# Kernel tuning notes

Measured on AMD Instinct MI355X. Metric: run time of the kernel, lower is better.

## Reference

```python
import jax, jax.numpy as jnp
import numpy as np

BT, L, F, N = 8, 8192, 128, 16


def setup_inputs() -> dict:
    key = jax.random.key(0)
    ks = jax.random.split(key, 7)
    scale = 1.0 / np.sqrt(F)
    x = jax.random.normal(ks[0], (BT, L, F), dtype=jnp.float32)
    Wb = jax.random.normal(ks[1], (F, N), dtype=jnp.float32) * scale
    bb = jax.random.normal(ks[2], (N,), dtype=jnp.float32) * 0.01
    Wc = jax.random.normal(ks[3], (F, N), dtype=jnp.float32) * scale
    bc = jax.random.normal(ks[4], (N,), dtype=jnp.float32) * 0.01
    Wd = jax.random.normal(ks[5], (F, 1), dtype=jnp.float32) * scale
    bd = jax.random.normal(ks[6], (1,), dtype=jnp.float32) * 0.01
    # diagonal HiPPO-like spectrum (A is diagonal in the source: torch.diag(eigenvalues))
    A = -(jnp.arange(N, dtype=jnp.float32) + 1.0)
    return {"x": x, "Wb": Wb, "bb": bb, "Wc": Wc, "bc": bc, "Wd": Wd, "bd": bd, "A": A}


def reference(x, Wb, bb, Wc, bc, Wd, bd, A):
    # input-dependent SSM parameters (S6 / selective scan)
    B = x @ Wb + bb                      # [BT, L, N]
    C = x @ Wc + bc                      # [BT, L, N]
    delta = jax.nn.softplus(x @ Wd + bd)  # [BT, L, 1]
    # ZOH discretization with diagonal A
    dA = jnp.exp(delta * A)              # [BT, L, N]
    dB = (dA - 1.0) / A * B              # [BT, L, N]

    def step(h, inp):
        dA_t, dB_t, x_t, C_t = inp       # [BT,N],[BT,N],[BT,F],[BT,N]
        # h: [BT, F, N]; each feature channel has its own N-dim state
        h = dA_t[:, None, :] * h + dB_t[:, None, :] * x_t[:, :, None]
        y = jnp.einsum('bfn,bn->bf', h, C_t)
        return h, y

    h0 = jnp.zeros((x.shape[0], x.shape[2], A.shape[0]), dtype=x.dtype)
    xs = (jnp.swapaxes(dA, 0, 1), jnp.swapaxes(dB, 0, 1),
          jnp.swapaxes(x, 0, 1), jnp.swapaxes(C, 0, 1))
    _, ys = jax.lax.scan(step, h0, xs)   # ys: [L, BT, F]
    return jnp.swapaxes(ys, 0, 1)        # [BT, L, F]
```

## Files before the change

kernel.cpp:

```cpp
#include <hip/hip_runtime.h>


#define BTc   8
#define Lseq  8192
#define Fdim  128
#define Ndim  16
#define CH    128
#define LC    64

__global__ __launch_bounds__(256) void k_pre(
    const float* __restrict__ x,
    const float* __restrict__ Wb, const float* __restrict__ bb,
    const float* __restrict__ Wc, const float* __restrict__ bc,
    const float* __restrict__ Wd, const float* __restrict__ bd,
    const float* __restrict__ A,  float* __restrict__ G)
{
    __shared__ float Wl[33][128];
    int tid = threadIdx.x;
    for (int idx = tid; idx < 33 * 128; idx += 256) {
        int j = idx >> 7, k = idx & 127;
        float v;
        if (j < 16)      v = Wb[k * 16 + j];
        else if (j < 32) v = Wc[k * 16 + (j - 16)];
        else             v = Wd[k];
        Wl[j][k] = v;
    }
    __syncthreads();

    int token = blockIdx.x * 256 + tid;
    const float* xr = x + (size_t)token * 128;

    float acc[33];
#pragma unroll
    for (int j = 0; j < 33; j++) acc[j] = 0.f;

#pragma unroll 2
    for (int kk = 0; kk < 32; kk++) {
        float4 xv = reinterpret_cast<const float4*>(xr)[kk];
#pragma unroll
        for (int j = 0; j < 33; j++) {
            float4 w = *reinterpret_cast<const float4*>(&Wl[j][kk * 4]);
            acc[j] = fmaf(xv.x, w.x, acc[j]);
            acc[j] = fmaf(xv.y, w.y, acc[j]);
            acc[j] = fmaf(xv.z, w.z, acc[j]);
            acc[j] = fmaf(xv.w, w.w, acc[j]);
        }
    }

    float v = acc[32] + bd[0];
    float delta = fmaxf(v, 0.f) + log1pf(expf(-fabsf(v)));

    float out[48];
#pragma unroll
    for (int n = 0; n < 16; n++) {
        float An = A[n];
        float Bn = acc[n] + bb[n];
        float Cn = acc[16 + n] + bc[n];
        float dA = expf(delta * An);
        float dB = (dA - 1.f) / An * Bn;
        out[n]      = dA;
        out[16 + n] = dB;
        out[32 + n] = Cn;
    }
    float4* Gr = reinterpret_cast<float4*>(G + (size_t)token * 48);
#pragma unroll
    for (int q = 0; q < 12; q++)
        Gr[q] = make_float4(out[4*q], out[4*q+1], out[4*q+2], out[4*q+3]);
}

__global__ __launch_bounds__(128) void k_local(
    const float* __restrict__ x, const float* __restrict__ G,
    float* __restrict__ q, float* __restrict__ P)
{
    __shared__ float Gl[LC][48];
    int c = blockIdx.x, b = blockIdx.y;
    int f = threadIdx.x;
    int t0 = c * LC;
    const float* Gc = G + (size_t)(b * Lseq + t0) * 48;
    for (int idx = f; idx < LC * 48 / 4; idx += 128)
        reinterpret_cast<float4*>(&Gl[0][0])[idx] =
            reinterpret_cast<const float4*>(Gc)[idx];
    __syncthreads();

    float h[16], pr[16];
#pragma unroll
    for (int n = 0; n < 16; n++) { h[n] = 0.f; pr[n] = 1.f; }

    const float* xp = x + (size_t)(b * Lseq + t0) * 128 + f;
    for (int t = 0; t < LC; t++) {
        float xv = xp[t * 128];
#pragma unroll
        for (int n = 0; n < 16; n++) {
            float dA = Gl[t][n];
            float dB = Gl[t][16 + n];
            h[n]  = fmaf(dA, h[n], dB * xv);
            pr[n] *= dA;
        }
    }

    float* qp = q + ((size_t)(b * CH + c) * 128 + f) * 16;
#pragma unroll
    for (int n = 0; n < 16; n++) qp[n] = h[n];
    if (f == 0) {
        float* Pp = P + (size_t)(b * CH + c) * 16;
#pragma unroll
        for (int n = 0; n < 16; n++) Pp[n] = pr[n];
    }
}

__global__ __launch_bounds__(256) void k_chunkscan(
    const float* __restrict__ q, const float* __restrict__ P,
    float* __restrict__ Hin)
{
    int id = blockIdx.x * 256 + threadIdx.x;
    int b  = id >> 11;
    int fn = id & 2047;
    int n  = id & 15;
    float H = 0.f;
    for (int c = 0; c < CH; c++) {
        size_t base = (size_t)(b * CH + c);
        Hin[base * 2048 + fn] = H;
        float Pc = P[base * 16 + n];
        float qc = q[base * 2048 + fn];
        H = fmaf(Pc, H, qc);
    }
}

__global__ __launch_bounds__(128) void k_final(
    const float* __restrict__ x, const float* __restrict__ G,
    const float* __restrict__ Hin, float* __restrict__ y)
{
    __shared__ float Gl[LC][48];
    int c = blockIdx.x, b = blockIdx.y;
    int f = threadIdx.x;
    int t0 = c * LC;
    const float* Gc = G + (size_t)(b * Lseq + t0) * 48;
    for (int idx = f; idx < LC * 48 / 4; idx += 128)
        reinterpret_cast<float4*>(&Gl[0][0])[idx] =
            reinterpret_cast<const float4*>(Gc)[idx];
    __syncthreads();

    float h[16];
    const float* hp = Hin + ((size_t)(b * CH + c) * 128 + f) * 16;
#pragma unroll
    for (int n = 0; n < 16; n++) h[n] = hp[n];

    const float* xp = x + (size_t)(b * Lseq + t0) * 128 + f;
    float*       yp = y + (size_t)(b * Lseq + t0) * 128 + f;
    for (int t = 0; t < LC; t++) {
        float xv  = xp[t * 128];
        float acc = 0.f;
#pragma unroll
        for (int n = 0; n < 16; n++) {
            float dA = Gl[t][n];
            float dB = Gl[t][16 + n];
            float Cn = Gl[t][32 + n];
            h[n] = fmaf(dA, h[n], dB * xv);
            acc  = fmaf(Cn, h[n], acc);
        }
        yp[t * 128] = acc;
    }
}

extern "C" void kernel_launch(void* const* d_in, const int* in_sizes, int n_in,
                              void* d_out, int out_size, void* d_ws, size_t ws_size,
                              hipStream_t stream) {
    const float* x  = (const float*)d_in[0];
    const float* Wb = (const float*)d_in[1];
    const float* bb = (const float*)d_in[2];
    const float* Wc = (const float*)d_in[3];
    const float* bc = (const float*)d_in[4];
    const float* Wd = (const float*)d_in[5];
    const float* bd = (const float*)d_in[6];
    const float* A  = (const float*)d_in[7];
    float* y = (float*)d_out;

    float* G   = (float*)d_ws;
    float* q   = G   + (size_t)BTc * Lseq * 48;
    float* P   = q   + (size_t)BTc * CH * Fdim * Ndim;
    float* Hin = P   + (size_t)BTc * CH * Ndim;

    k_pre<<<dim3(BTc * Lseq / 256), 256, 0, stream>>>(x, Wb, bb, Wc, bc, Wd, bd, A, G);
    k_local<<<dim3(CH, BTc), 128, 0, stream>>>(x, G, q, P);
    k_chunkscan<<<dim3(BTc * Fdim * Ndim / 256), 256, 0, stream>>>(q, P, Hin);
    k_final<<<dim3(CH, BTc), 128, 0, stream>>>(x, G, Hin, y);
}
```

Measured before the change: 95.84 us.

## Fuse projection with local chunk scan and replace final rescan with linear correction

New measurement: 119.6 us. 1.25x slower.

```diff
diff --git a/kernel.cpp b/kernel.cpp
--- a/kernel.cpp
+++ b/kernel.cpp
@@ -8,15 +8,29 @@
 #define CH    128
 #define LC    64
 
-__global__ __launch_bounds__(256) void k_pre(
+__global__ __launch_bounds__(256) void k_fused_local(
     const float* __restrict__ x,
     const float* __restrict__ Wb, const float* __restrict__ bb,
     const float* __restrict__ Wc, const float* __restrict__ bc,
     const float* __restrict__ Wd, const float* __restrict__ bd,
-    const float* __restrict__ A,  float* __restrict__ G)
+    const float* __restrict__ A,
+    float* __restrict__ y,
+    float* __restrict__ q, float* __restrict__ P, float* __restrict__ E)
 {
+    __shared__ float Xl[LC][132];
     __shared__ float Wl[33][128];
-    int tid = threadIdx.x;
+    __shared__ float Gl[LC][48];
+    __shared__ float El[LC][16];
+
+    const int tid = threadIdx.x;
+    const int c = blockIdx.x, b = blockIdx.y;
+    const size_t tok0 = (size_t)b * Lseq + (size_t)c * LC;
+
+    const float4* xg = reinterpret_cast<const float4*>(x + tok0 * Fdim);
+    for (int idx = tid; idx < LC * 32; idx += 256) {
+        int t = idx >> 5, k4 = idx & 31;
+        *reinterpret_cast<float4*>(&Xl[t][k4 * 4]) = xg[idx];
+    }
     for (int idx = tid; idx < 33 * 128; idx += 256) {
         int j = idx >> 7, k = idx & 127;
         float v;
@@ -27,84 +41,80 @@
     }
     __syncthreads();
 
-    int token = blockIdx.x * 256 + tid;
-    const float* xr = x + (size_t)token * 128;
-
-    float acc[33];
-#pragma unroll
-    for (int j = 0; j < 33; j++) acc[j] = 0.f;
-
-#pragma unroll 2
-    for (int kk = 0; kk < 32; kk++) {
-        float4 xv = reinterpret_cast<const float4*>(xr)[kk];
-#pragma unroll
-        for (int j = 0; j < 33; j++) {
-            float4 w = *reinterpret_cast<const float4*>(&Wl[j][kk * 4]);
-            acc[j] = fmaf(xv.x, w.x, acc[j]);
-            acc[j] = fmaf(xv.y, w.y, acc[j]);
-            acc[j] = fmaf(xv.z, w.z, acc[j]);
-            acc[j] = fmaf(xv.w, w.w, acc[j]);
-        }
-    }
-
-    float v = acc[32] + bd[0];
-    float delta = fmaxf(v, 0.f) + log1pf(expf(-fabsf(v)));
-
-    float out[48];
-#pragma unroll
-    for (int n = 0; n < 16; n++) {
-        float An = A[n];
-        float Bn = acc[n] + bb[n];
-        float Cn = acc[16 + n] + bc[n];
-        float dA = expf(delta * An);
-        float dB = (dA - 1.f) / An * Bn;
-        out[n]      = dA;
-        out[16 + n] = dB;
-        out[32 + n] = Cn;
-    }
-    float4* Gr = reinterpret_cast<float4*>(G + (size_t)token * 48);
-#pragma unroll
-    for (int q = 0; q < 12; q++)
-        Gr[q] = make_float4(out[4*q], out[4*q+1], out[4*q+2], out[4*q+3]);
-}
-
-__global__ __launch_bounds__(128) void k_local(
-    const float* __restrict__ x, const float* __restrict__ G,
-    float* __restrict__ q, float* __restrict__ P)
-{
-    __shared__ float Gl[LC][48];
-    int c = blockIdx.x, b = blockIdx.y;
-    int f = threadIdx.x;
-    int t0 = c * LC;
-    const float* Gc = G + (size_t)(b * Lseq + t0) * 48;
-    for (int idx = f; idx < LC * 48 / 4; idx += 128)
-        reinterpret_cast<float4*>(&Gl[0][0])[idx] =
-            reinterpret_cast<const float4*>(Gc)[idx];
-    __syncthreads();
-
-    float h[16], pr[16];
-#pragma unroll
-    for (int n = 0; n < 16; n++) { h[n] = 0.f; pr[n] = 1.f; }
-
-    const float* xp = x + (size_t)(b * Lseq + t0) * 128 + f;
-    for (int t = 0; t < LC; t++) {
-        float xv = xp[t * 128];
-#pragma unroll
-        for (int n = 0; n < 16; n++) {
-            float dA = Gl[t][n];
-            float dB = Gl[t][16 + n];
-            h[n]  = fmaf(dA, h[n], dB * xv);
-            pr[n] *= dA;
-        }
-    }
-
-    float* qp = q + ((size_t)(b * CH + c) * 128 + f) * 16;
-#pragma unroll
-    for (int n = 0; n < 16; n++) qp[n] = h[n];
-    if (f == 0) {
-        float* Pp = P + (size_t)(b * CH + c) * 16;
-#pragma unroll
-        for (int n = 0; n < 16; n++) Pp[n] = pr[n];
+    {
+        const int t = tid >> 2, ks = tid & 3;
+        float acc[33];
+#pragma unroll
+        for (int j = 0; j < 33; ++j) acc[j] = 0.f;
+#pragma unroll
+        for (int kk = 0; kk < 8; ++kk) {
+            float4 xv = *reinterpret_cast<const float4*>(&Xl[t][ks * 32 + kk * 4]);
+#pragma unroll
+            for (int j = 0; j < 33; ++j) {
+                float4 w = *reinterpret_cast<const float4*>(&Wl[j][ks * 32 + kk * 4]);
+                acc[j] = fmaf(xv.x, w.x, acc[j]);
+                acc[j] = fmaf(xv.y, w.y, acc[j]);
+                acc[j] = fmaf(xv.z, w.z, acc[j]);
+                acc[j] = fmaf(xv.w, w.w, acc[j]);
+            }
+        }
+#pragma unroll
+        for (int j = 0; j < 33; ++j) {
+            acc[j] += __shfl_xor(acc[j], 1);
+            acc[j] += __shfl_xor(acc[j], 2);
+        }
+        if (ks == 0) {
+            float v = acc[32] + bd[0];
+            float delta = fmaxf(v, 0.f) + log1pf(expf(-fabsf(v)));
+#pragma unroll
+            for (int n = 0; n < 16; ++n) {
+                float An = A[n];
+                float dA = expf(delta * An);
+                float dB = (dA - 1.f) / An * (acc[n] + bb[n]);
+                Gl[t][n]      = dA;
+                Gl[t][16 + n] = dB;
+                Gl[t][32 + n] = acc[16 + n] + bc[n];
+            }
+        }
+    }
+    __syncthreads();
+
+    if (tid < 16) {
+        const int n = tid;
+        float cum = 1.f;
+        for (int t = 0; t < LC; ++t) {
+            cum *= Gl[t][n];
+            El[t][n] = cum * Gl[t][32 + n];
+        }
+        P[(size_t)(b * CH + c) * 16 + n] = cum;
+    }
+    __syncthreads();
+
+    if (tid < 128) {
+        const int f = tid;
+        float h[16];
+#pragma unroll
+        for (int n = 0; n < 16; ++n) h[n] = 0.f;
+        float* yp = y + tok0 * Fdim + f;
+        for (int t = 0; t < LC; ++t) {
+            float xv = Xl[t][f];
+            float yacc = 0.f;
+#pragma unroll
+            for (int n = 0; n < 16; ++n) {
+                h[n] = fmaf(Gl[t][n], h[n], Gl[t][16 + n] * xv);
+                yacc = fmaf(Gl[t][32 + n], h[n], yacc);
+            }
+            yp[t * Fdim] = yacc;
+        }
+        float4* qp = reinterpret_cast<float4*>(q + ((size_t)(b * CH + c) * 128 + f) * 16);
+#pragma unroll
+        for (int n4 = 0; n4 < 4; ++n4)
+            qp[n4] = make_float4(h[4*n4], h[4*n4+1], h[4*n4+2], h[4*n4+3]);
+    } else {
+        float4* Eg = reinterpret_cast<float4*>(E + (size_t)(b * CH + c) * LC * 16);
+        const float4* Es = reinterpret_cast<const float4*>(&El[0][0]);
+        for (int idx = tid - 128; idx < LC * 16 / 4; idx += 128)
+            Eg[idx] = Es[idx];
     }
 }
 
@@ -117,48 +127,51 @@
     int fn = id & 2047;
     int n  = id & 15;
     float H = 0.f;
-    for (int c = 0; c < CH; c++) {
-        size_t base = (size_t)(b * CH + c);
-        Hin[base * 2048 + fn] = H;
-        float Pc = P[base * 16 + n];
-        float qc = q[base * 2048 + fn];
-        H = fmaf(Pc, H, qc);
-    }
-}
-
-__global__ __launch_bounds__(128) void k_final(
-    const float* __restrict__ x, const float* __restrict__ G,
-    const float* __restrict__ Hin, float* __restrict__ y)
+    size_t qb = (size_t)b * CH * 2048 + fn;
+    size_t pb = (size_t)b * CH * 16 + n;
+    for (int cg = 0; cg < CH; cg += 16) {
+        float Pr[16], qr[16];
+#pragma unroll
+        for (int i = 0; i < 16; ++i) {
+            Pr[i] = P[pb + (size_t)(cg + i) * 16];
+            qr[i] = q[qb + (size_t)(cg + i) * 2048];
+        }
+#pragma unroll
+        for (int i = 0; i < 16; ++i) {
+            Hin[qb + (size_t)(cg + i) * 2048] = H;
+            H = fmaf(Pr[i], H, qr[i]);
+        }
+    }
+}
+
+__global__ __launch_bounds__(128) void k_correct(
+    const float* __restrict__ Hin, const float* __restrict__ E,
+    float* __restrict__ y)
 {
-    __shared__ float Gl[LC][48];
-    int c = blockIdx.x, b = blockIdx.y;
-    int f = threadIdx.x;
-    int t0 = c * LC;
-    const float* Gc = G + (size_t)(b * Lseq + t0) * 48;
-    for (int idx = f; idx < LC * 48 / 4; idx += 128)
-        reinterpret_cast<float4*>(&Gl[0][0])[idx] =
-            reinterpret_cast<const float4*>(Gc)[idx];
-    __syncthreads();
-
-    float h[16];
-    const float* hp = Hin + ((size_t)(b * CH + c) * 128 + f) * 16;
-#pragma unroll
-    for (int n = 0; n < 16; n++) h[n] = hp[n];
-
-    const float* xp = x + (size_t)(b * Lseq + t0) * 128 + f;
-    float*       yp = y + (size_t)(b * Lseq + t0) * 128 + f;
-    for (int t = 0; t < LC; t++) {
-        float xv  = xp[t * 128];
+    __shared__ float El[LC][16];
+    const int c = blockIdx.x, b = blockIdx.y;
+    const int f = threadIdx.x;
+
+    const float4* Eg = reinterpret_cast<const float4*>(E + (size_t)(b * CH + c) * LC * 16);
+    float4* Es = reinterpret_cast<float4*>(&El[0][0]);
+    for (int idx = f; idx < LC * 16 / 4; idx += 128) Es[idx] = Eg[idx];
+
+    float hv[16];
+    const float4* hp = reinterpret_cast<const float4*>(Hin + ((size_t)(b * CH + c) * 128 + f) * 16);
+#pragma unroll
+    for (int n4 = 0; n4 < 4; ++n4) {
+        float4 v = hp[n4];
+        hv[4*n4] = v.x; hv[4*n4+1] = v.y; hv[4*n4+2] = v.z; hv[4*n4+3] = v.w;
+    }
+    __syncthreads();
+
+    float* yp = y + ((size_t)b * Lseq + (size_t)c * LC) * Fdim + f;
+#pragma unroll 8
+    for (int t = 0; t < LC; ++t) {
         float acc = 0.f;
 #pragma unroll
-        for (int n = 0; n < 16; n++) {
-            float dA = Gl[t][n];
-            float dB = Gl[t][16 + n];
-            float Cn = Gl[t][32 + n];
-            h[n] = fmaf(dA, h[n], dB * xv);
-            acc  = fmaf(Cn, h[n], acc);
-        }
-        yp[t * 128] = acc;
+        for (int n = 0; n < 16; ++n) acc = fmaf(El[t][n], hv[n], acc);
+        yp[t * Fdim] += acc;
     }
 }
 
@@ -175,13 +188,13 @@
     const float* A  = (const float*)d_in[7];
     float* y = (float*)d_out;
 
-    float* G   = (float*)d_ws;
-    float* q   = G   + (size_t)BTc * Lseq * 48;
+    float* q   = (float*)d_ws;
     float* P   = q   + (size_t)BTc * CH * Fdim * Ndim;
     float* Hin = P   + (size_t)BTc * CH * Ndim;
-
-    k_pre<<<dim3(BTc * Lseq / 256), 256, 0, stream>>>(x, Wb, bb, Wc, bc, Wd, bd, A, G);
-    k_local<<<dim3(CH, BTc), 128, 0, stream>>>(x, G, q, P);
+    float* E   = Hin + (size_t)BTc * CH * Fdim * Ndim;
+
+    k_fused_local<<<dim3(CH, BTc), 256, 0, stream>>>(x, Wb, bb, Wc, bc, Wd, bd, A,
+                                                     y, q, P, E);
     k_chunkscan<<<dim3(BTc * Fdim * Ndim / 256), 256, 0, stream>>>(q, P, Hin);
-    k_final<<<dim3(CH, BTc), 128, 0, stream>>>(x, G, Hin, y);
-}
+    k_correct<<<dim3(CH, BTc), 128, 0, stream>>>(Hin, E, y);
+}
```
